# Kernel optimization log

Measured on AMD Instinct MI355X. Metric: run time of the kernel, lower is better.

## Reference

```python
import math
import jax, jax.numpy as jnp
import numpy as np

EPS = 1.0
B, T, D, H = 8, 512, 768, 12
DH = D // H  # 64


def setup_inputs() -> dict:
    key = jax.random.key(0)
    ks = jax.random.split(key, 10)
    std = 0.02
    return {
        "x": jax.random.normal(ks[0], (B, T, D), dtype=jnp.float32),
        "r_position_embedding": jax.random.normal(ks[1], (T, D), dtype=jnp.float32),
        "r_content_bias": jax.random.normal(ks[2], (H, DH), dtype=jnp.float32),
        "r_position_bias": jax.random.normal(ks[3], (H, DH), dtype=jnp.float32),
        # Conv1D(linear) params, stored as (in, out) so y = x @ W + b
        "Wqkv": jax.random.normal(ks[4], (D, 3 * D), dtype=jnp.float32) * std,
        "bqkv": jnp.zeros((3 * D,), dtype=jnp.float32),
        "Wh": jax.random.normal(ks[5], (D, D), dtype=jnp.float32) * std,
        "bh": jnp.zeros((D,), dtype=jnp.float32),
        "Wp": jax.random.normal(ks[6], (D, D), dtype=jnp.float32) * std,
        "bp": jnp.zeros((D,), dtype=jnp.float32),
    }


def reference(x, r_position_embedding, r_content_bias, r_position_bias,
              Wqkv, bqkv, Wh, bh, Wp, bp):
    # QKV projection and head split
    qkv = x @ Wqkv + bqkv                                   # (B,T,3D)
    q, k, v = jnp.split(qkv, 3, axis=-1)
    split_heads = lambda t: t.reshape(B, T, H, DH).transpose(0, 2, 1, 3)  # (B,H,T,DH)
    q, k, v = split_heads(q), split_heads(k), split_heads(v)

    # content scores
    scores = jnp.einsum('bhtd,bhsd->bhts', q, k)            # (B,H,T,T)

    # relative position projection: linear is row-wise, so project once then gather.
    # rel_pos[c, r] = linear_position(pos_emb[max(0, c - r)])
    proj = (r_position_embedding @ Wp + bp).reshape(T, H, DH)  # (P=T, H, DH)
    idx = jnp.maximum(0, jnp.arange(T)[:, None] - jnp.arange(T)[None, :])  # (T,T) = max(0, c-r)

    # q . rel_pos term: compute vs all P distinct positions, then gather per (c, r)
    rel_q = jnp.einsum('bhtd,phd->bhtp', q, proj)           # (B,H,T,P)
    scores = scores + jnp.take_along_axis(rel_q, idx[None, None, :, :], axis=-1)

    # content-bias and position-bias terms (query-independent)
    bias_c = jnp.einsum('hd,phd->hp', r_content_bias, proj)[:, idx]   # (H,T,T)
    bias_p = jnp.einsum('hd,phd->hp', r_position_bias, proj)[:, idx]  # (H,T,T)
    scores = scores + bias_c[None] + bias_p[None]

    # masked softmax with EPS=1 quirks (faithful to original)
    scores = scores / (math.sqrt(DH) + EPS)
    mask = jnp.tril(jnp.ones((T, T), dtype=jnp.float32))    # causal
    masked_exps = jnp.exp(scores) * mask
    att = masked_exps / (masked_exps.sum(-1, keepdims=True) + 2.0 * EPS)

    ctx = jnp.einsum('bhts,bhsd->bhtd', att, v)             # (B,H,T,DH)
    # original: permute(0,2,3,1) then flatten -> (B,T,DH*H) interleaving (d, h)
    ctx = ctx.transpose(0, 2, 3, 1).reshape(B, T, D)
    out = ctx @ Wh + bh
    k_out = k.transpose(0, 1, 3, 2)                         # (B,H,DH,T) as module returns
    return out, k_out, v
```

## Files before the change

kernel.cpp:

```cpp
#include <hip/hip_runtime.h>
#include <hip/hip_bf16.h>


#define NT 512
#define ND 768
#define NH 12

typedef short short4_t __attribute__((ext_vector_type(4)));
typedef short short8_t __attribute__((ext_vector_type(8)));
typedef float float4_t __attribute__((ext_vector_type(4)));

__device__ __forceinline__ float b2f(unsigned short u) {
    union { unsigned int i; float f; } x; x.i = ((unsigned int)u) << 16; return x.f;
}
__device__ __forceinline__ unsigned short f2b(float f) {
    union { float f; unsigned int i; } x; x.f = f;
    unsigned int i = x.i;
    i += 0x7fffu + ((i >> 16) & 1u);
    return (unsigned short)(i >> 16);
}

__global__ __launch_bounds__(256) void prep(
    const float* __restrict__ x, unsigned short* __restrict__ xb,
    const float* __restrict__ Wqkv, unsigned short* __restrict__ WqkvT,
    const float* __restrict__ Wh, unsigned short* __restrict__ WhT)
{
    __shared__ float t[32][33];
    const int bid = blockIdx.x;
    const int tid = threadIdx.x;

    if (bid < 1536) {
        const int i = bid * 256 + tid;
        const float* s = x + (size_t)i * 8;
        float4_t f0 = *(const float4_t*)s;
        float4_t f1 = *(const float4_t*)(s + 4);
        union { short8_t v; unsigned short u[8]; } pk;
        pk.u[0] = f2b(f0[0]); pk.u[1] = f2b(f0[1]); pk.u[2] = f2b(f0[2]); pk.u[3] = f2b(f0[3]);
        pk.u[4] = f2b(f1[0]); pk.u[5] = f2b(f1[1]); pk.u[6] = f2b(f1[2]); pk.u[7] = f2b(f1[3]);
        *(short8_t*)&xb[(size_t)i * 8] = pk.v;
        return;
    }
    const float* in; unsigned short* out; int K, N, k0, n0;
    if (bid < 3264) {
        const int tt = bid - 1536;
        in = Wqkv; out = WqkvT; K = 768; N = 2304;
        n0 = (tt % 72) * 32; k0 = (tt / 72) * 32;
    } else {
        const int tt = bid - 3264;
        in = Wh; out = WhT; K = 768; N = 768;
        n0 = (tt % 24) * 32; k0 = (tt / 24) * 32;
    }
    const int r = tid >> 3;
    const int c = (tid & 7) * 4;
    float4_t v = *(const float4_t*)&in[(size_t)(k0 + r) * N + n0 + c];
    t[r][c + 0] = v[0]; t[r][c + 1] = v[1]; t[r][c + 2] = v[2]; t[r][c + 3] = v[3];
    __syncthreads();
    union { short4_t v; unsigned short u[4]; } pk;
    pk.u[0] = f2b(t[c + 0][r]);
    pk.u[1] = f2b(t[c + 1][r]);
    pk.u[2] = f2b(t[c + 2][r]);
    pk.u[3] = f2b(t[c + 3][r]);
    *(short4_t*)&out[(size_t)(n0 + r) * K + k0 + c] = pk.v;
}

__global__ __launch_bounds__(256) void gemm_qkv(
    const unsigned short* __restrict__ A, const unsigned short* __restrict__ BT,
    const float* __restrict__ biasf,
    unsigned short* __restrict__ ob0, float* __restrict__ o1, float* __restrict__ o2,
    unsigned short* __restrict__ sh1, unsigned short* __restrict__ sh2)
{
    __shared__ __attribute__((aligned(16))) unsigned short Al[128 * 32];
    __shared__ __attribute__((aligned(16))) unsigned short Bl[128 * 32];

    const int K    = 768;
    const int tid  = threadIdx.x;
    int qb = blockIdx.x;
    qb = (qb & 7) * 72 + (qb >> 3);
    const int m0   = (qb / 18) * 128;
    const int n0   = (qb % 18) * 128;
    const int wave = tid >> 6;
    const int lane = tid & 63;
    const int lm   = lane & 15;
    const int quad = lane >> 4;
    const int wr   = (wave >> 1) * 64;
    const int wc   = (wave & 1) * 64;

    float4_t acc[4][4];
#pragma unroll
    for (int mt = 0; mt < 4; ++mt)
#pragma unroll
        for (int nt = 0; nt < 4; ++nt)
#pragma unroll
            for (int r = 0; r < 4; ++r) acc[mt][nt][r] = 0.f;

    const unsigned short* ap = A  + (size_t)(m0 + (tid >> 2)) * K + (tid & 3) * 8;
    const unsigned short* bp = BT + (size_t)(n0 + (tid >> 2)) * K + (tid & 3) * 8;
    const size_t rstep = (size_t)64 * K;
    unsigned short* al0 = Al + wave * 512;
    unsigned short* bl0 = Bl + wave * 512;

    for (int k0 = 0; k0 < K; k0 += 32) {
        if (k0) __syncthreads();
        __builtin_amdgcn_global_load_lds(
            (const __attribute__((address_space(1))) void*)(ap + k0),
            (__attribute__((address_space(3))) void*)al0, 16, 0, 0);
        __builtin_amdgcn_global_load_lds(
            (const __attribute__((address_space(1))) void*)(ap + rstep + k0),
            (__attribute__((address_space(3))) void*)(al0 + 2048), 16, 0, 0);
        __builtin_amdgcn_global_load_lds(
            (const __attribute__((address_space(1))) void*)(bp + k0),
            (__attribute__((address_space(3))) void*)bl0, 16, 0, 0);
        __builtin_amdgcn_global_load_lds(
            (const __attribute__((address_space(1))) void*)(bp + rstep + k0),
            (__attribute__((address_space(3))) void*)(bl0 + 2048), 16, 0, 0);
        __syncthreads();

        short8_t af[4], bf[4];
#pragma unroll
        for (int mt = 0; mt < 4; ++mt)
            af[mt] = *(const short8_t*)&Al[(wr + mt * 16 + lm) * 32 + quad * 8];
#pragma unroll
        for (int nt = 0; nt < 4; ++nt)
            bf[nt] = *(const short8_t*)&Bl[(wc + nt * 16 + lm) * 32 + quad * 8];
#pragma unroll
        for (int mt = 0; mt < 4; ++mt)
#pragma unroll
            for (int nt = 0; nt < 4; ++nt)
                acc[mt][nt] = __builtin_amdgcn_mfma_f32_16x16x32_bf16(af[mt], bf[nt], acc[mt][nt], 0, 0, 0);
    }

    const int sec = n0 / 768;
#pragma unroll
    for (int nt = 0; nt < 4; ++nt) {
        const int gcol = n0 + wc + nt * 16 + lm;
        const int cc = gcol - sec * 768;
        const int h = cc >> 6, d = cc & 63;
        const float bv = biasf[gcol];
#pragma unroll
        for (int mt = 0; mt < 4; ++mt) {
#pragma unroll
            for (int r = 0; r < 4; ++r) {
                const int grow = m0 + wr + mt * 16 + quad * 4 + r;
                const int b = grow >> 9, t = grow & 511;
                const float val = acc[mt][nt][r] + bv;
                if (sec == 0) {
                    ob0[((size_t)((b * NH + h) * NT + t)) * 64 + d] = f2b(val);
                } else if (sec == 1) {
                    o1[((size_t)((b * NH + h) * 64 + d)) * NT + t] = val;
                    sh1[((size_t)((b * NH + h) * NT + t)) * 64 + d] = f2b(val);
                } else {
                    o2[((size_t)((b * NH + h) * NT + t)) * 64 + d] = val;
                    sh2[((size_t)((b * NH + h) * 64 + d)) * NT + t] = f2b(val);
                }
            }
        }
    }
}

__global__ __launch_bounds__(256) void gemm_proj(
    const float* __restrict__ Af, const float* __restrict__ Bw,
    const float* __restrict__ biasf,
    const float* __restrict__ rcb, const float* __restrict__ rpb,
    unsigned short* __restrict__ projb, float* __restrict__ biascp)
{
    __shared__ unsigned short Al[64][40];
    __shared__ unsigned short Bl[64][40];

    const int tid  = threadIdx.x;
    const int m0   = blockIdx.y * 64;
    const int n0   = blockIdx.x * 64;
    const int wave = tid >> 6;
    const int lane = tid & 63;
    const int lm   = lane & 15;
    const int quad = lane >> 4;
    const int koff = quad * 8;
    const int K = 768, ldb = 768;

    float4_t acc[4];
#pragma unroll
    for (int j = 0; j < 4; ++j)
#pragma unroll
        for (int r = 0; r < 4; ++r) acc[j][r] = 0.0f;

    const int arow = tid >> 2;
    const int acg  = (tid & 3) * 8;
    const int bk   = tid & 31;
    const int bg   = tid >> 5;

    for (int k0 = 0; k0 < K; k0 += 32) {
        {
            const float* src = &Af[(size_t)(m0 + arow) * K + k0 + acg];
            float4_t f0 = *(const float4_t*)src;
            float4_t f1 = *(const float4_t*)(src + 4);
            union { short8_t v; unsigned short u[8]; } pk;
            pk.u[0] = f2b(f0[0]); pk.u[1] = f2b(f0[1]); pk.u[2] = f2b(f0[2]); pk.u[3] = f2b(f0[3]);
            pk.u[4] = f2b(f1[0]); pk.u[5] = f2b(f1[1]); pk.u[6] = f2b(f1[2]); pk.u[7] = f2b(f1[3]);
            *(short8_t*)&Al[arow][acg] = pk.v;
        }
        {
            const float* src = &Bw[(size_t)(k0 + bk) * ldb + n0 + bg * 8];
            float4_t f0 = *(const float4_t*)src;
            float4_t f1 = *(const float4_t*)(src + 4);
            Bl[bg * 8 + 0][bk] = f2b(f0[0]); Bl[bg * 8 + 1][bk] = f2b(f0[1]);
            Bl[bg * 8 + 2][bk] = f2b(f0[2]); Bl[bg * 8 + 3][bk] = f2b(f0[3]);
            Bl[bg * 8 + 4][bk] = f2b(f1[0]); Bl[bg * 8 + 5][bk] = f2b(f1[1]);
            Bl[bg * 8 + 6][bk] = f2b(f1[2]); Bl[bg * 8 + 7][bk] = f2b(f1[3]);
        }
        __syncthreads();

        short8_t af = *(const short8_t*)&Al[wave * 16 + lm][koff];
#pragma unroll
        for (int j = 0; j < 4; ++j) {
            short8_t bf = *(const short8_t*)&Bl[j * 16 + lm][koff];
            acc[j] = __builtin_amdgcn_mfma_f32_16x16x32_bf16(af, bf, acc[j], 0, 0, 0);
        }
        __syncthreads();
    }

    const int h = n0 >> 6;
    float cb4[4], part[4] = {0.f, 0.f, 0.f, 0.f};
#pragma unroll
    for (int j = 0; j < 4; ++j) {
        const int d = j * 16 + lm;
        cb4[j] = rcb[h * 64 + d] + rpb[h * 64 + d];
    }
#pragma unroll
    for (int j = 0; j < 4; ++j) {
        const int gcol = n0 + j * 16 + lm;
        const int d = gcol & 63;
        const float bv = biasf[gcol];
#pragma unroll
        for (int r = 0; r < 4; ++r) {
            const int grow = m0 + wave * 16 + quad * 4 + r;
            const float val = acc[j][r] + bv;
            projb[((size_t)(h * NT + grow)) * 64 + d] = f2b(val);
            part[r] += val * cb4[j];
        }
    }
#pragma unroll
    for (int r = 0; r < 4; ++r) {
        float v = part[r];
        v += __shfl_xor(v, 1); v += __shfl_xor(v, 2);
        v += __shfl_xor(v, 4); v += __shfl_xor(v, 8);
        if (lm == 0) biascp[h * NT + m0 + wave * 16 + quad * 4 + r] = v;
    }
}

__global__ __launch_bounds__(256) void gemm_out(
    const unsigned short* __restrict__ A, const unsigned short* __restrict__ BT,
    const float* __restrict__ biasf, float* __restrict__ o1)
{
    __shared__ __attribute__((aligned(16))) unsigned short Al[3][64 * 32];
    __shared__ __attribute__((aligned(16))) unsigned short Bl[3][128 * 32];

    const int K    = 768;
    const int tid  = threadIdx.x;
    const int bid  = (blockIdx.x & 7) * 48 + (blockIdx.x >> 3);
    const int wave = tid >> 6;
    const int lane = tid & 63;
    const int lm   = lane & 15;
    const int quad = lane >> 4;
    const int wr   = (wave >> 1) * 32;
    const int wc   = (wave & 1) * 64;

    const int m0 = (bid / 6) * 64;
    const int n0 = (bid % 6) * 128;

    float4_t acc[2][4];
#pragma unroll
    for (int mt = 0; mt < 2; ++mt)
#pragma unroll
        for (int nt = 0; nt < 4; ++nt)
#pragma unroll
            for (int r = 0; r < 4; ++r) acc[mt][nt][r] = 0.f;

    const unsigned short* ap = A  + (size_t)(m0 + (tid >> 2)) * K + (tid & 3) * 8;
    const unsigned short* bp = BT + (size_t)(n0 + (tid >> 2)) * K + (tid & 3) * 8;
    const size_t rstep = (size_t)64 * K;

    auto stage = [&](int bi, int k0) {
        unsigned short* al0 = &Al[bi][0] + wave * 512;
        unsigned short* bl0 = &Bl[bi][0] + wave * 512;
        __builtin_amdgcn_global_load_lds(
            (const __attribute__((address_space(1))) void*)(ap + k0),
            (__attribute__((address_space(3))) void*)al0, 16, 0, 0);
        __builtin_amdgcn_global_load_lds(
            (const __attribute__((address_space(1))) void*)(bp + k0),
            (__attribute__((address_space(3))) void*)bl0, 16, 0, 0);
        __builtin_amdgcn_global_load_lds(
            (const __attribute__((address_space(1))) void*)(bp + rstep + k0),
            (__attribute__((address_space(3))) void*)(bl0 + 2048), 16, 0, 0);
    };

    stage(0, 0);
    stage(1, 32);

    int cur = 0;
    for (int k0 = 0; k0 < K; k0 += 32) {
        if (k0 + 32 < K) asm volatile("s_waitcnt vmcnt(3)" ::: "memory");
        else             asm volatile("s_waitcnt vmcnt(0)" ::: "memory");
        __builtin_amdgcn_s_barrier();
        __builtin_amdgcn_sched_barrier(0);

        if (k0 + 64 < K) stage((cur + 2) % 3, k0 + 64);

        short8_t af[2], bf[4];
#pragma unroll
        for (int mt = 0; mt < 2; ++mt)
            af[mt] = *(const short8_t*)&Al[cur][(wr + mt * 16 + lm) * 32 + quad * 8];
#pragma unroll
        for (int nt = 0; nt < 4; ++nt)
            bf[nt] = *(const short8_t*)&Bl[cur][(wc + nt * 16 + lm) * 32 + quad * 8];
#pragma unroll
        for (int mt = 0; mt < 2; ++mt)
#pragma unroll
            for (int nt = 0; nt < 4; ++nt)
                acc[mt][nt] = __builtin_amdgcn_mfma_f32_16x16x32_bf16(af[mt], bf[nt], acc[mt][nt], 0, 0, 0);

        cur = (cur + 1) % 3;
    }

#pragma unroll
    for (int nt = 0; nt < 4; ++nt) {
        const int gcol = n0 + wc + nt * 16 + lm;
        const float bv = biasf[gcol];
#pragma unroll
        for (int mt = 0; mt < 2; ++mt)
#pragma unroll
            for (int r = 0; r < 4; ++r) {
                const int grow = m0 + wr + mt * 16 + quad * 4 + r;
                o1[(size_t)grow * ND + gcol] = acc[mt][nt][r] + bv;
            }
    }
}

__global__ __launch_bounds__(128) void attn_mfma(
    const unsigned short* __restrict__ q_ws, const unsigned short* __restrict__ k_ws,
    const unsigned short* __restrict__ v_ws, const unsigned short* __restrict__ projb,
    const float* __restrict__ biascp, unsigned short* __restrict__ ctxT)
{
    __shared__ unsigned short Kt[64][72];
    __shared__ unsigned short Vt[64][72];
    __shared__ unsigned short pP[96][72];
    __shared__ float          Rl[2][16][84];
    __shared__ unsigned short esl[2][16][72];

    const int tid   = threadIdx.x;
    const int y     = blockIdx.y;
    const int h     = y % NH;
    const int b     = y / NH;
    const int pairi = blockIdx.x;
    const int wave  = tid >> 6;
    const int lane  = tid & 63;
    const int lm    = lane & 15;
    const int quad  = lane >> 4;
    const int koff  = quad * 8;

    const int sr = tid >> 1;
    const int sc = (tid & 1) * 32;

    for (int c = 0; c < 2; ++c) {
        const int ti  = c ? pairi : (15 - pairi);
        const int tb0 = ti * 32;
        const int tw0 = tb0 + wave * 16;
        const int nst = (tb0 >> 6) + 1;

        short8_t aq[2];
        aq[0] = *(const short8_t*)&q_ws[((size_t)(y * NT + tw0 + lm)) * 64 + koff];
        aq[1] = *(const short8_t*)&q_ws[((size_t)(y * NT + tw0 + lm)) * 64 + koff + 32];

        float4_t ctxacc[4];
#pragma unroll
        for (int j = 0; j < 4; ++j)
#pragma unroll
            for (int r = 0; r < 4; ++r) ctxacc[j][r] = 0.f;
        float esum[4] = {0.f, 0.f, 0.f, 0.f};

        for (int st = 0; st < nst; ++st) {
            const int s0      = st * 64;
            const int plo_blk = max(0, tb0 - s0 - 63);
            const int cnt_blk = tb0 + 31 - s0 - plo_blk + 1;
            if (c | st) __syncthreads();
            {
                const unsigned short* ks = &k_ws[((size_t)(y * NT + s0 + sr)) * 64 + sc];
                *(short8_t*)&Kt[sr][sc]      = *(const short8_t*)ks;
                *(short8_t*)&Kt[sr][sc + 8]  = *(const short8_t*)(ks + 8);
                *(short8_t*)&Kt[sr][sc + 16] = *(const short8_t*)(ks + 16);
                *(short8_t*)&Kt[sr][sc + 24] = *(const short8_t*)(ks + 24);
                const unsigned short* vs = &v_ws[((size_t)(y * 64 + sr)) * NT + s0 + sc];
                *(short8_t*)&Vt[sr][sc]      = *(const short8_t*)vs;
                *(short8_t*)&Vt[sr][sc + 8]  = *(const short8_t*)(vs + 8);
                *(short8_t*)&Vt[sr][sc + 16] = *(const short8_t*)(vs + 16);
                *(short8_t*)&Vt[sr][sc + 24] = *(const short8_t*)(vs + 24);
                for (int p = tid; p < cnt_blk; p += 128) {
                    const unsigned short* ps = &projb[((size_t)(h * NT + plo_blk + p)) * 64];
                    *(short8_t*)&pP[p][0]  = *(const short8_t*)ps;
                    *(short8_t*)&pP[p][8]  = *(const short8_t*)(ps + 8);
                    *(short8_t*)&pP[p][16] = *(const short8_t*)(ps + 16);
                    *(short8_t*)&pP[p][24] = *(const short8_t*)(ps + 24);
                    *(short8_t*)&pP[p][32] = *(const short8_t*)(ps + 32);
                    *(short8_t*)&pP[p][40] = *(const short8_t*)(ps + 40);
                    *(short8_t*)&pP[p][48] = *(const short8_t*)(ps + 48);
                    *(short8_t*)&pP[p][56] = *(const short8_t*)(ps + 56);
                }
            }
            __syncthreads();

            if (s0 <= tw0 + 15) {
                const int plo_w = max(0, tw0 - s0 - 63);
                const int pbase = plo_w - plo_blk;
                const int cntw  = tw0 + 15 - s0 - plo_w + 1;
                const int jmax  = min(3, (tw0 + 15 - s0) >> 4);
                const int jpmax = (cntw - 1) >> 4;

                float4_t accQK[4];
#pragma unroll
                for (int j = 0; j < 4; ++j)
#pragma unroll
                    for (int r = 0; r < 4; ++r) accQK[j][r] = 0.f;
                for (int j = 0; j <= jmax; ++j) {
                    short8_t bk0 = *(const short8_t*)&Kt[j * 16 + lm][koff];
                    short8_t bk1 = *(const short8_t*)&Kt[j * 16 + lm][koff + 32];
                    accQK[j] = __builtin_amdgcn_mfma_f32_16x16x32_bf16(aq[0], bk0, accQK[j], 0, 0, 0);
                    accQK[j] = __builtin_amdgcn_mfma_f32_16x16x32_bf16(aq[1], bk1, accQK[j], 0, 0, 0);
                }
                for (int j = 0; j <= jpmax; ++j) {
                    short8_t bp0 = *(const short8_t*)&pP[pbase + j * 16 + lm][koff];
                    short8_t bp1 = *(const short8_t*)&pP[pbase + j * 16 + lm][koff + 32];
                    float4_t accR;
#pragma unroll
                    for (int r = 0; r < 4; ++r) accR[r] = 0.f;
                    accR = __builtin_amdgcn_mfma_f32_16x16x32_bf16(aq[0], bp0, accR, 0, 0, 0);
                    accR = __builtin_amdgcn_mfma_f32_16x16x32_bf16(aq[1], bp1, accR, 0, 0, 0);
                    const int p = j * 16 + lm;
                    const float bv = biascp[h * NT + min(plo_w + p, NT - 1)];
#pragma unroll
                    for (int r = 0; r < 4; ++r) Rl[wave][quad * 4 + r][p] = accR[r] + bv;
                }
                asm volatile("" ::: "memory");

#pragma unroll
                for (int j = 0; j < 4; ++j) {
                    const int s_g = s0 + j * 16 + lm;
#pragma unroll
                    for (int r = 0; r < 4; ++r) {
                        const int t_g = tw0 + quad * 4 + r;
                        float e = 0.f;
                        if (s_g <= t_g) {
                            const int p = t_g - s_g - plo_w;
                            e = __expf(fminf((accQK[j][r] + Rl[wave][quad * 4 + r][p]) * (1.f / 9.f), 60.f));
                        }
                        esl[wave][quad * 4 + r][j * 16 + lm] = f2b(e);
                        esum[r] += e;
                    }
                }
                asm volatile("" ::: "memory");

                short8_t ae0 = *(const short8_t*)&esl[wave][lm][koff];
                short8_t ae1 = *(const short8_t*)&esl[wave][lm][koff + 32];
#pragma unroll
                for (int j = 0; j < 4; ++j) {
                    short8_t bv0 = *(const short8_t*)&Vt[j * 16 + lm][koff];
                    short8_t bv1 = *(const short8_t*)&Vt[j * 16 + lm][koff + 32];
                    ctxacc[j] = __builtin_amdgcn_mfma_f32_16x16x32_bf16(ae0, bv0, ctxacc[j], 0, 0, 0);
                    ctxacc[j] = __builtin_amdgcn_mfma_f32_16x16x32_bf16(ae1, bv1, ctxacc[j], 0, 0, 0);
                }
            }
        }

        float rcpv[4];
#pragma unroll
        for (int r = 0; r < 4; ++r) {
            float v = esum[r];
            v += __shfl_xor(v, 1); v += __shfl_xor(v, 2);
            v += __shfl_xor(v, 4); v += __shfl_xor(v, 8);
            rcpv[r] = 1.f / (v + 2.f);
        }
#pragma unroll
        for (int j = 0; j < 4; ++j) {
            const int d = j * 16 + lm;
#pragma unroll
            for (int r = 0; r < 4; ++r) {
                const int t = tw0 + quad * 4 + r;
                ctxT[((size_t)(b * NT + t)) * ND + d * NH + h] = f2b(ctxacc[j][r] * rcpv[r]);
            }
        }
    }
}

extern "C" void kernel_launch(void* const* d_in, const int* in_sizes, int n_in,
                              void* d_out, int out_size, void* d_ws, size_t ws_size,
                              hipStream_t stream)
{
    const float* x    = (const float*)d_in[0];
    const float* rpe  = (const float*)d_in[1];
    const float* rcb  = (const float*)d_in[2];
    const float* rpb  = (const float*)d_in[3];
    const float* Wqkv = (const float*)d_in[4];
    const float* bqkv = (const float*)d_in[5];
    const float* Wh   = (const float*)d_in[6];
    const float* bh   = (const float*)d_in[7];
    const float* Wp   = (const float*)d_in[8];
    const float* bp   = (const float*)d_in[9];

    float* out  = (float*)d_out;
    float* kout = out + 3145728;
    float* vout = out + 6291456;

    unsigned short* q_ws  = (unsigned short*)d_ws;
    unsigned short* k_ws  = q_ws + 3145728;
    unsigned short* v_ws  = k_ws + 3145728;
    unsigned short* ctxT  = v_ws + 3145728;
    unsigned short* xb    = ctxT;
    unsigned short* projb = ctxT + 3145728;
    float* biascp = (float*)(projb + 393216);
    unsigned short* WqkvT = (unsigned short*)(biascp + 6144);
    unsigned short* WhT   = WqkvT + 1769472;

    prep<<<dim3(3840), 256, 0, stream>>>(x, xb, Wqkv, WqkvT, Wh, WhT);

    gemm_qkv<<<dim3(576), 256, 0, stream>>>(
        xb, WqkvT, bqkv, q_ws, kout, vout, k_ws, v_ws);
    gemm_proj<<<dim3(768 / 64, 512 / 64), 256, 0, stream>>>(
        rpe, Wp, bp, rcb, rpb, projb, biascp);
    attn_mfma<<<dim3(8, 96), 128, 0, stream>>>(
        q_ws, k_ws, v_ws, projb, biascp, ctxT);
    gemm_out<<<dim3(384), 256, 0, stream>>>(
        ctxT, WhT, bh, out);
}
```

Baseline: 218.1 us.

## Fold position projection GEMM into prep kernel and remap attention blocks per XCD

```diff
diff --git a/kernel.cpp b/kernel.cpp
--- a/kernel.cpp
+++ b/kernel.cpp
@@ -23,14 +23,101 @@
 __global__ __launch_bounds__(256) void prep(
     const float* __restrict__ x, unsigned short* __restrict__ xb,
     const float* __restrict__ Wqkv, unsigned short* __restrict__ WqkvT,
-    const float* __restrict__ Wh, unsigned short* __restrict__ WhT)
+    const float* __restrict__ Wh, unsigned short* __restrict__ WhT,
+    const float* __restrict__ rpe, const float* __restrict__ Wp,
+    const float* __restrict__ bp, const float* __restrict__ rcb,
+    const float* __restrict__ rpb, unsigned short* __restrict__ projb,
+    float* __restrict__ biascp)
 {
     __shared__ float t[32][33];
+    __shared__ unsigned short Al[64][40];
+    __shared__ unsigned short Bl[64][40];
     const int bid = blockIdx.x;
     const int tid = threadIdx.x;
 
-    if (bid < 1536) {
-        const int i = bid * 256 + tid;
+    if (bid < 96) {
+        const int m0   = (bid / 12) * 64;
+        const int n0   = (bid % 12) * 64;
+        const int wave = tid >> 6;
+        const int lane = tid & 63;
+        const int lm   = lane & 15;
+        const int quad = lane >> 4;
+        const int koff = quad * 8;
+        const int K = 768, ldb = 768;
+
+        float4_t acc[4];
+#pragma unroll
+        for (int j = 0; j < 4; ++j)
+#pragma unroll
+            for (int r = 0; r < 4; ++r) acc[j][r] = 0.0f;
+
+        const int arow = tid >> 2;
+        const int acg  = (tid & 3) * 8;
+        const int bk   = tid & 31;
+        const int bg   = tid >> 5;
+
+        for (int k0 = 0; k0 < K; k0 += 32) {
+            {
+                const float* src = &rpe[(size_t)(m0 + arow) * K + k0 + acg];
+                float4_t f0 = *(const float4_t*)src;
+                float4_t f1 = *(const float4_t*)(src + 4);
+                union { short8_t v; unsigned short u[8]; } pk;
+                pk.u[0] = f2b(f0[0]); pk.u[1] = f2b(f0[1]); pk.u[2] = f2b(f0[2]); pk.u[3] = f2b(f0[3]);
+                pk.u[4] = f2b(f1[0]); pk.u[5] = f2b(f1[1]); pk.u[6] = f2b(f1[2]); pk.u[7] = f2b(f1[3]);
+                *(short8_t*)&Al[arow][acg] = pk.v;
+            }
+            {
+                const float* src = &Wp[(size_t)(k0 + bk) * ldb + n0 + bg * 8];
+                float4_t f0 = *(const float4_t*)src;
+                float4_t f1 = *(const float4_t*)(src + 4);
+                Bl[bg * 8 + 0][bk] = f2b(f0[0]); Bl[bg * 8 + 1][bk] = f2b(f0[1]);
+                Bl[bg * 8 + 2][bk] = f2b(f0[2]); Bl[bg * 8 + 3][bk] = f2b(f0[3]);
+                Bl[bg * 8 + 4][bk] = f2b(f1[0]); Bl[bg * 8 + 5][bk] = f2b(f1[1]);
+                Bl[bg * 8 + 6][bk] = f2b(f1[2]); Bl[bg * 8 + 7][bk] = f2b(f1[3]);
+            }
+            __syncthreads();
+
+            short8_t af = *(const short8_t*)&Al[wave * 16 + lm][koff];
+#pragma unroll
+            for (int j = 0; j < 4; ++j) {
+                short8_t bf = *(const short8_t*)&Bl[j * 16 + lm][koff];
+                acc[j] = __builtin_amdgcn_mfma_f32_16x16x32_bf16(af, bf, acc[j], 0, 0, 0);
+            }
+            __syncthreads();
+        }
+
+        const int h = n0 >> 6;
+        float cb4[4], part[4] = {0.f, 0.f, 0.f, 0.f};
+#pragma unroll
+        for (int j = 0; j < 4; ++j) {
+            const int d = j * 16 + lm;
+            cb4[j] = rcb[h * 64 + d] + rpb[h * 64 + d];
+        }
+#pragma unroll
+        for (int j = 0; j < 4; ++j) {
+            const int gcol = n0 + j * 16 + lm;
+            const int d = gcol & 63;
+            const float bv = bp[gcol];
+#pragma unroll
+            for (int r = 0; r < 4; ++r) {
+                const int grow = m0 + wave * 16 + quad * 4 + r;
+                const float val = acc[j][r] + bv;
+                projb[((size_t)(h * NT + grow)) * 64 + d] = f2b(val);
+                part[r] += val * cb4[j];
+            }
+        }
+#pragma unroll
+        for (int r = 0; r < 4; ++r) {
+            float v = part[r];
+            v += __shfl_xor(v, 1); v += __shfl_xor(v, 2);
+            v += __shfl_xor(v, 4); v += __shfl_xor(v, 8);
+            if (lm == 0) biascp[h * NT + m0 + wave * 16 + quad * 4 + r] = v;
+        }
+        return;
+    }
+
+    if (bid < 1632) {
+        const int i = (bid - 96) * 256 + tid;
         const float* s = x + (size_t)i * 8;
         float4_t f0 = *(const float4_t*)s;
         float4_t f1 = *(const float4_t*)(s + 4);
@@ -41,12 +128,12 @@
         return;
     }
     const float* in; unsigned short* out; int K, N, k0, n0;
-    if (bid < 3264) {
-        const int tt = bid - 1536;
+    if (bid < 3360) {
+        const int tt = bid - 1632;
         in = Wqkv; out = WqkvT; K = 768; N = 2304;
         n0 = (tt % 72) * 32; k0 = (tt / 72) * 32;
     } else {
-        const int tt = bid - 3264;
+        const int tt = bid - 3360;
         in = Wh; out = WhT; K = 768; N = 768;
         n0 = (tt % 24) * 32; k0 = (tt / 24) * 32;
     }
@@ -157,95 +244,6 @@
     }
 }
 
-__global__ __launch_bounds__(256) void gemm_proj(
-    const float* __restrict__ Af, const float* __restrict__ Bw,
-    const float* __restrict__ biasf,
-    const float* __restrict__ rcb, const float* __restrict__ rpb,
-    unsigned short* __restrict__ projb, float* __restrict__ biascp)
-{
-    __shared__ unsigned short Al[64][40];
-    __shared__ unsigned short Bl[64][40];
-
-    const int tid  = threadIdx.x;
-    const int m0   = blockIdx.y * 64;
-    const int n0   = blockIdx.x * 64;
-    const int wave = tid >> 6;
-    const int lane = tid & 63;
-    const int lm   = lane & 15;
-    const int quad = lane >> 4;
-    const int koff = quad * 8;
-    const int K = 768, ldb = 768;
-
-    float4_t acc[4];
-#pragma unroll
-    for (int j = 0; j < 4; ++j)
-#pragma unroll
-        for (int r = 0; r < 4; ++r) acc[j][r] = 0.0f;
-
-    const int arow = tid >> 2;
-    const int acg  = (tid & 3) * 8;
-    const int bk   = tid & 31;
-    const int bg   = tid >> 5;
-
-    for (int k0 = 0; k0 < K; k0 += 32) {
-        {
-            const float* src = &Af[(size_t)(m0 + arow) * K + k0 + acg];
-            float4_t f0 = *(const float4_t*)src;
-            float4_t f1 = *(const float4_t*)(src + 4);
-            union { short8_t v; unsigned short u[8]; } pk;
-            pk.u[0] = f2b(f0[0]); pk.u[1] = f2b(f0[1]); pk.u[2] = f2b(f0[2]); pk.u[3] = f2b(f0[3]);
-            pk.u[4] = f2b(f1[0]); pk.u[5] = f2b(f1[1]); pk.u[6] = f2b(f1[2]); pk.u[7] = f2b(f1[3]);
-            *(short8_t*)&Al[arow][acg] = pk.v;
-        }
-        {
-            const float* src = &Bw[(size_t)(k0 + bk) * ldb + n0 + bg * 8];
-            float4_t f0 = *(const float4_t*)src;
-            float4_t f1 = *(const float4_t*)(src + 4);
-            Bl[bg * 8 + 0][bk] = f2b(f0[0]); Bl[bg * 8 + 1][bk] = f2b(f0[1]);
-            Bl[bg * 8 + 2][bk] = f2b(f0[2]); Bl[bg * 8 + 3][bk] = f2b(f0[3]);
-            Bl[bg * 8 + 4][bk] = f2b(f1[0]); Bl[bg * 8 + 5][bk] = f2b(f1[1]);
-            Bl[bg * 8 + 6][bk] = f2b(f1[2]); Bl[bg * 8 + 7][bk] = f2b(f1[3]);
-        }
-        __syncthreads();
-
-        short8_t af = *(const short8_t*)&Al[wave * 16 + lm][koff];
-#pragma unroll
-        for (int j = 0; j < 4; ++j) {
-            short8_t bf = *(const short8_t*)&Bl[j * 16 + lm][koff];
-            acc[j] = __builtin_amdgcn_mfma_f32_16x16x32_bf16(af, bf, acc[j], 0, 0, 0);
-        }
-        __syncthreads();
-    }
-
-    const int h = n0 >> 6;
-    float cb4[4], part[4] = {0.f, 0.f, 0.f, 0.f};
-#pragma unroll
-    for (int j = 0; j < 4; ++j) {
-        const int d = j * 16 + lm;
-        cb4[j] = rcb[h * 64 + d] + rpb[h * 64 + d];
-    }
-#pragma unroll
-    for (int j = 0; j < 4; ++j) {
-        const int gcol = n0 + j * 16 + lm;
-        const int d = gcol & 63;
-        const float bv = biasf[gcol];
-#pragma unroll
-        for (int r = 0; r < 4; ++r) {
-            const int grow = m0 + wave * 16 + quad * 4 + r;
-            const float val = acc[j][r] + bv;
-            projb[((size_t)(h * NT + grow)) * 64 + d] = f2b(val);
-            part[r] += val * cb4[j];
-        }
-    }
-#pragma unroll
-    for (int r = 0; r < 4; ++r) {
-        float v = part[r];
-        v += __shfl_xor(v, 1); v += __shfl_xor(v, 2);
-        v += __shfl_xor(v, 4); v += __shfl_xor(v, 8);
-        if (lm == 0) biascp[h * NT + m0 + wave * 16 + quad * 4 + r] = v;
-    }
-}
-
 __global__ __launch_bounds__(256) void gemm_out(
     const unsigned short* __restrict__ A, const unsigned short* __restrict__ BT,
     const float* __restrict__ biasf, float* __restrict__ o1)
@@ -346,10 +344,13 @@
     __shared__ unsigned short esl[2][16][72];
 
     const int tid   = threadIdx.x;
-    const int y     = blockIdx.y;
+    const int bid   = blockIdx.x;
+    const int xcd   = bid & 7;
+    const int jj    = bid >> 3;
+    const int y     = xcd * 12 + (jj >> 3);
+    const int pairi = jj & 7;
     const int h     = y % NH;
     const int b     = y / NH;
-    const int pairi = blockIdx.x;
     const int wave  = tid >> 6;
     const int lane  = tid & 63;
     const int lm    = lane & 15;
@@ -517,13 +518,12 @@
     unsigned short* WqkvT = (unsigned short*)(biascp + 6144);
     unsigned short* WhT   = WqkvT + 1769472;
 
-    prep<<<dim3(3840), 256, 0, stream>>>(x, xb, Wqkv, WqkvT, Wh, WhT);
+    prep<<<dim3(3936), 256, 0, stream>>>(x, xb, Wqkv, WqkvT, Wh, WhT,
+                                         rpe, Wp, bp, rcb, rpb, projb, biascp);
 
     gemm_qkv<<<dim3(576), 256, 0, stream>>>(
         xb, WqkvT, bqkv, q_ws, kout, vout, k_ws, v_ws);
-    gemm_proj<<<dim3(768 / 64, 512 / 64), 256, 0, stream>>>(
-        rpe, Wp, bp, rcb, rpb, projb, biascp);
-    attn_mfma<<<dim3(8, 96), 128, 0, stream>>>(
+    attn_mfma<<<dim3(768), 128, 0, stream>>>(
         q_ws, k_ws, v_ws, projb, biascp, ctxT);
     gemm_out<<<dim3(384), 256, 0, stream>>>(
         ctxT, WhT, bh, out);
```

After: 211.1 us. 3.2% less time.
